# Kernel optimization log

Hardware: AMD Instinct MI355X
Metric: run time of the kernel (lower is better)

The kernel has to match this reference:

```python
import jax, jax.numpy as jnp
import numpy as np

B, N, K, D, H = 32, 4096, 8, 256, 512
ITERS = 3
LN_EPS = 1e-5  # torch LayerNorm default; self.eps is unused in forward


def _ln(x, g, b):
    m = jnp.mean(x, axis=-1, keepdims=True)
    v = jnp.mean(jnp.square(x - m), axis=-1, keepdims=True)
    return (x - m) * jax.lax.rsqrt(v + LN_EPS) * g + b


def setup_inputs() -> dict:
    key = jax.random.key(0)
    ks = jax.random.split(key, 16)
    s = 0.02
    return {
        "inputs": jax.random.normal(ks[0], (B, N, D), jnp.float32),
        "slots_init": jax.random.normal(ks[1], (B, K, D), jnp.float32),
        "ln_in_g": jnp.ones((D,), jnp.float32), "ln_in_b": jnp.zeros((D,), jnp.float32),
        "ln_s_g": jnp.ones((D,), jnp.float32), "ln_s_b": jnp.zeros((D,), jnp.float32),
        "ln_ff_g": jnp.ones((D,), jnp.float32), "ln_ff_b": jnp.zeros((D,), jnp.float32),
        "Wk": s * jax.random.normal(ks[2], (D, D), jnp.float32), "bk": jnp.zeros((D,), jnp.float32),
        "Wq": s * jax.random.normal(ks[3], (D, D), jnp.float32), "bq": jnp.zeros((D,), jnp.float32),
        "Wv": s * jax.random.normal(ks[4], (D, D), jnp.float32), "bv": jnp.zeros((D,), jnp.float32),
        "W_ih": s * jax.random.normal(ks[5], (3 * D, D), jnp.float32),
        "b_ih": jnp.zeros((3 * D,), jnp.float32),
        "W_hh": s * jax.random.normal(ks[6], (3 * D, D), jnp.float32),
        "b_hh": jnp.zeros((3 * D,), jnp.float32),
        "W1": s * jax.random.normal(ks[7], (H, D), jnp.float32), "b1": jnp.zeros((H,), jnp.float32),
        "W2": s * jax.random.normal(ks[8], (D, H), jnp.float32), "b2": jnp.zeros((D,), jnp.float32),
    }


def _gru_cell(x, h, W_ih, b_ih, W_hh, b_hh):
    # PyTorch GRUCell: gates in order r, z, n
    gi = x @ W_ih.T + b_ih  # [*, 3D]
    gh = h @ W_hh.T + b_hh
    ir, iz, inn = jnp.split(gi, 3, axis=-1)
    hr, hz, hn = jnp.split(gh, 3, axis=-1)
    r = jax.nn.sigmoid(ir + hr)
    z = jax.nn.sigmoid(iz + hz)
    n = jnp.tanh(inn + r * hn)
    return (1.0 - z) * n + z * h


def reference(inputs, slots_init, ln_in_g, ln_in_b, ln_s_g, ln_s_b, ln_ff_g, ln_ff_b,
              Wk, bk, Wq, bq, Wv, bv, W_ih, b_ih, W_hh, b_hh, W1, b1, W2, b2):
    d = inputs.shape[-1]
    x = _ln(inputs, ln_in_g, ln_in_b)  # [B,N,D]
    # k, v depend only on x; hoisted out of the loop (same math as source)
    k = x @ Wk.T + bk                  # project_inputs
    v = x @ Wv.T + bv                  # project_v
    scale = 1.0 / jnp.sqrt(jnp.asarray(d, inputs.dtype))
    slots = slots_init
    for _ in range(ITERS):
        slots_prev = slots
        q = _ln(slots, ln_s_g, ln_s_b) @ Wq.T + bq          # [B,K,D]
        attn_logits = jnp.einsum('bkd,bnd->bkn', q, k) * scale
        # competitive softmax over the SLOT axis (dim=1), not keys
        attn = jax.nn.softmax(attn_logits, axis=1)          # [B,K,N]
        updates = jnp.einsum('bkn,bnd->bkd', attn, v)
        slots = _gru_cell(updates, slots_prev, W_ih, b_ih, W_hh, b_hh)
        hdd = jax.nn.relu(_ln(slots, ln_ff_g, ln_ff_b) @ W1.T + b1)
        slots = slots + hdd @ W2.T + b2
    return slots
```

## Files before the change

### kernel.cpp

```cpp
#include <hip/hip_runtime.h>
#include <hip/hip_bf16.h>
#include <cstddef>
#include <cstdint>

#define BB 32
#define NN 4096
#define KK 8
#define DD 256
#define HH 512
#define LN_EPS 1e-5f
#define SCALE 0.0625f
#define NCHUNK 32

__device__ __forceinline__ float wave_sum(float v) {
#pragma unroll
  for (int off = 32; off >= 1; off >>= 1) v += __shfl_xor(v, off);
  return v;
}

__device__ __forceinline__ float sigmoidf_(float x) { return 1.0f / (1.0f + __expf(-x)); }

#define OFF_G   0
#define OFF_W1  393216
#define OFF_W2  524288
#define OFF_WV  655360
#define OFF_WQ  720896
#define OFF_WK  786432
#define WB_ELEMS 851968

#define G_PRE (BB * KK)
#define G_W2B (512 * 11)
#define G_SETUP (G_PRE + G_W2B + 1)

__device__ __forceinline__ float dotp4(uint2 w, float4 s) {
  return __uint_as_float(w.x << 16) * s.x + __uint_as_float(w.x & 0xffff0000u) * s.y +
         __uint_as_float(w.y << 16) * s.z + __uint_as_float(w.y & 0xffff0000u) * s.w;
}

template <int OUT, int KL>
__device__ __forceinline__ float gemv_p(const ushort* __restrict__ wt, int j, int kb,
                                        const float* __restrict__ src) {
  const uint2* p = (const uint2*)(wt + ((size_t)(kb >> 2) * OUT + j) * 4);
  float a = 0.0f;
#pragma unroll 16
  for (int e = 0; e < KL / 4; ++e) {
    uint2 w = p[(size_t)e * OUT];
    float4 s = *(const float4*)(src + kb + e * 4);
    a += dotp4(w, s);
  }
  return a;
}

__global__ __launch_bounds__(256) void k_setup(
    const float* __restrict__ Wih, const float* __restrict__ Whh,
    const float* __restrict__ W1, const float* __restrict__ W2,
    const float* __restrict__ Wv, const float* __restrict__ Wq,
    const float* __restrict__ Wk, ushort* __restrict__ wb,
    const float* __restrict__ slots, const float* __restrict__ gs, const float* __restrict__ bs,
    const float* __restrict__ bq, const float* __restrict__ bk,
    const float* __restrict__ gi, const float* __restrict__ bi,
    const float* __restrict__ bv, float* __restrict__ bvw,
    float* __restrict__ qk, float* __restrict__ qb) {
  int blk = blockIdx.x;
  if (blk < G_PRE) {
    int row = blk;
    int t = threadIdx.x;
    int wid = t >> 6, lane = t & 63;
    __shared__ float lns[DD];
    __shared__ float qs[DD];
    __shared__ float rb[8];
    float sv = slots[(size_t)row * DD + t];
    float s = wave_sum(sv);
    float s2 = wave_sum(sv * sv);
    if (lane == 0) { rb[wid] = s; rb[4 + wid] = s2; }
    __syncthreads();
    float tot = rb[0] + rb[1] + rb[2] + rb[3];
    float tot2 = rb[4] + rb[5] + rb[6] + rb[7];
    float m = tot * (1.0f / DD);
    float var = tot2 * (1.0f / DD) - m * m;
    float rs = rsqrtf(var + LN_EPS);
    lns[t] = (sv - m) * rs * gs[t] + bs[t];
    __syncthreads();
    float acc = 0.0f;
    const float4* wr = (const float4*)(Wq + (size_t)t * DD);
#pragma unroll 4
    for (int e4 = 0; e4 < DD / 4; ++e4) {
      float4 w = wr[e4];
      float4 l = ((const float4*)lns)[e4];
      acc += w.x * l.x + w.y * l.y + w.z * l.z + w.w * l.w;
    }
    qs[t] = acc + bq[t];
    __syncthreads();
    float a2 = 0.0f;
    for (int d = 0; d < DD; ++d) a2 = fmaf(qs[d], Wk[(size_t)d * DD + t], a2);
    float a2S = SCALE * a2;
    qk[(size_t)row * DD + t] = a2S * gi[t];
    float pb = wave_sum(qs[t] * bk[t]);
    float pb2 = wave_sum(a2S * bi[t]);
    __syncthreads();
    if (lane == 0) { rb[wid] = pb; rb[4 + wid] = pb2; }
    __syncthreads();
    if (t == 0) qb[row] = SCALE * (rb[0] + rb[1] + rb[2] + rb[3]) + rb[4] + rb[5] + rb[6] + rb[7];
  } else if (blk < G_PRE + G_W2B) {
    int q2 = blk - G_PRE;
    int m = q2 >> 9;
    int idx = (q2 & 511) * 256 + threadIdx.x;
    const int sizes[11] = {65536, 65536, 65536, 65536, 65536, 65536, 131072, 131072, 65536, 65536, 65536};
    const int offs[11] = {OFF_G, OFF_G + 65536, OFF_G + 131072, OFF_G + 196608, OFF_G + 262144,
                          OFF_G + 327680, OFF_W1, OFF_W2, OFF_WV, OFF_WQ, OFF_WK};
    if (idx >= sizes[m]) return;
    int K = (m == 7) ? 512 : 256;
    int OUT = (m == 6) ? 512 : 256;
    int k = idx % K, j = idx / K;
    float v;
    switch (m) {
      case 0: case 1: case 2: v = Wih[((size_t)(m * 256 + j)) * 256 + k]; break;
      case 3: case 4: case 5: v = Whh[((size_t)((m - 3) * 256 + j)) * 256 + k]; break;
      case 6: v = W1[(size_t)j * 256 + k]; break;
      case 7: v = W2[(size_t)j * 512 + k]; break;
      case 8: v = Wv[(size_t)j * 256 + k] * gi[k]; break;
      case 9: v = Wq[(size_t)j * 256 + k]; break;
      default: v = Wk[(size_t)k * 256 + j]; break;
    }
    __hip_bfloat16 h = __float2bfloat16(v);
    wb[(size_t)offs[m] + (size_t)(k >> 2) * OUT * 4 + j * 4 + (k & 3)] = *(ushort*)&h;
  } else {
    int t = threadIdx.x;
    float a = bv[t];
    const float4* wr = (const float4*)(Wv + (size_t)t * DD);
    const float4* bb = (const float4*)bi;
#pragma unroll 4
    for (int e4 = 0; e4 < DD / 4; ++e4) {
      float4 w = wr[e4];
      float4 x = bb[e4];
      a += w.x * x.x + w.y * x.y + w.z * x.z + w.w * x.w;
    }
    bvw[t] = a;
  }
}

template <int DO_LN>
__global__ __launch_bounds__(256, 2) void k_attn_t(const ushort* __restrict__ xb_in,
                                                   ushort* __restrict__ xb_out,
                                                   const float* __restrict__ inp,
                                                   const float* __restrict__ qk,
                                                   const float* __restrict__ qb,
                                                   float* __restrict__ uxp,
                                                   float* __restrict__ sap) {
  typedef __attribute__((ext_vector_type(8))) short short8;
  typedef __attribute__((ext_vector_type(4))) float f32x4;

  __shared__ __align__(16) ushort q_l[16 * 256];
  __shared__ __align__(16) ushort xt[4][32 * 256];

  int t = threadIdx.x, wid = t >> 6, lane = t & 63;
  int bI = blockIdx.x >> 5, c = blockIdx.x & 31;
  int lm = lane & 15, g = lane >> 4;
  ushort* xw = xt[wid];

  {
    const float* qkb = qk + (size_t)bI * (KK * DD);
#pragma unroll
    for (int s = 0; s < 16; ++s) {
      float qv = qkb[(s & 7) * 256 + t];
      __hip_bfloat16 hb = __float2bfloat16(qv);
      ushort st = *(ushort*)&hb;
      if (s >= 8) {
        float lo = qv - __bfloat162float(hb);
        __hip_bfloat16 lb2 = __float2bfloat16(lo);
        st = *(ushort*)&lb2;
      }
      int pos = (t >> 3) ^ (s & 7);
      q_l[s * 256 + pos * 8 + (t & 7)] = st;
    }
  }
  float qbv = qb[bI * 8 + (lane & 7)];
  __syncthreads();

  int row0 = c * 128 + wid * 32;

  if (DO_LN) {
    int q8 = lane & 7, lr = lane >> 3;
    const float* rp0 = inp + ((size_t)bI * NN + row0 + lr) * DD + q8 * 4;
    float4 cur[8];
#pragma unroll
    for (int i = 0; i < 8; ++i) cur[i] = *(const float4*)(rp0 + i * 32);
    for (int p = 0; p < 4; ++p) {
      float4 nxt[8];
      if (p < 3) {
#pragma unroll
        for (int i = 0; i < 8; ++i) nxt[i] = *(const float4*)(rp0 + (size_t)(p + 1) * 8 * DD + i * 32);
      }
      float s1 = 0.0f, s2 = 0.0f;
#pragma unroll
      for (int i = 0; i < 8; ++i) {
        s1 += cur[i].x + cur[i].y + cur[i].z + cur[i].w;
        s2 += cur[i].x * cur[i].x + cur[i].y * cur[i].y + cur[i].z * cur[i].z + cur[i].w * cur[i].w;
      }
      s1 += __shfl_xor(s1, 1); s2 += __shfl_xor(s2, 1);
      s1 += __shfl_xor(s1, 2); s2 += __shfl_xor(s2, 2);
      s1 += __shfl_xor(s1, 4); s2 += __shfl_xor(s2, 4);
      float m = s1 * (1.0f / DD);
      float var = s2 * (1.0f / DD) - m * m;
      float rs = rsqrtf(var + LN_EPS);
      int rr = p * 8 + lr;
      int hb2 = (q8 & 1) * 4;
#pragma unroll
      for (int i = 0; i < 8; ++i) {
        float y0 = (cur[i].x - m) * rs, y1 = (cur[i].y - m) * rs;
        float y2 = (cur[i].z - m) * rs, y3 = (cur[i].w - m) * rs;
        __hip_bfloat16 h0 = __float2bfloat16(y0), h1 = __float2bfloat16(y1);
        __hip_bfloat16 h2 = __float2bfloat16(y2), h3 = __float2bfloat16(y3);
        uint2 wv;
        wv.x = (uint)*(ushort*)&h0 | ((uint)*(ushort*)&h1 << 16);
        wv.y = (uint)*(ushort*)&h2 | ((uint)*(ushort*)&h3 << 16);
        int chunk = i * 4 + (q8 >> 1);
        *(uint2*)&xw[rr * DD + ((chunk ^ rr) << 3) + hb2] = wv;
      }
      if (p < 3) {
#pragma unroll
        for (int i = 0; i < 8; ++i) cur[i] = nxt[i];
      }
    }
    ushort* xbt = xb_out + ((size_t)bI * NN + row0) * DD;
#pragma unroll
    for (int i = 0; i < 16; ++i) {
      uint4 v = *(const uint4*)&xw[i * 512 + lane * 8];
      *(uint4*)&xbt[i * 512 + lane * 8] = v;
    }
  } else {
    const ushort* srcb = xb_in + ((size_t)bI * NN + row0) * DD;
#pragma unroll
    for (int i = 0; i < 16; ++i) {
      __builtin_amdgcn_global_load_lds(
          (__attribute__((address_space(1))) void*)(srcb + i * 512 + lane * 8),
          (__attribute__((address_space(3))) void*)&xw[i * 512], 16, 0, 0);
    }
    asm volatile("s_waitcnt vmcnt(0)" ::: "memory");
    __builtin_amdgcn_sched_barrier(0);
  }

  union V16 { uint4 u; short8 s; };
  int rA = lm, rB = lm + 16;
  f32x4 ac0 = {}, ac1 = {};
#pragma unroll
  for (int kk = 0; kk < 8; ++kk) {
    V16 qf, x0, x1;
    int ch = kk * 4 + g;
    qf.u = *(const uint4*)&q_l[lm * 256 + ((ch ^ (lm & 7)) << 3)];
    x0.u = *(const uint4*)&xw[rA * 256 + ((ch ^ rA) << 3)];
    x1.u = *(const uint4*)&xw[rB * 256 + ((ch ^ rB) << 3)];
    ac0 = __builtin_amdgcn_mfma_f32_16x16x32_bf16(x0.s, qf.s, ac0, 0, 0, 0);
    ac1 = __builtin_amdgcn_mfma_f32_16x16x32_bf16(x1.s, qf.s, ac1, 0, 0, 0);
  }

  float a0[4], a1[4];
  {
    float lv0[4], lv1[4], mx0[4], mx1[4], ss0[4], ss1[4];
#pragma unroll
    for (int r = 0; r < 4; ++r) {
      lv0[r] = ac0[r] + __shfl_xor(ac0[r], 8) + qbv;
      lv1[r] = ac1[r] + __shfl_xor(ac1[r], 8) + qbv;
      mx0[r] = lv0[r]; mx1[r] = lv1[r];
    }
#pragma unroll
    for (int off = 1; off <= 4; off <<= 1) {
#pragma unroll
      for (int r = 0; r < 4; ++r) {
        mx0[r] = fmaxf(mx0[r], __shfl_xor(mx0[r], off));
        mx1[r] = fmaxf(mx1[r], __shfl_xor(mx1[r], off));
      }
    }
#pragma unroll
    for (int r = 0; r < 4; ++r) {
      a0[r] = __expf(lv0[r] - mx0[r]);
      a1[r] = __expf(lv1[r] - mx1[r]);
      ss0[r] = a0[r]; ss1[r] = a1[r];
    }
#pragma unroll
    for (int off = 1; off <= 4; off <<= 1) {
#pragma unroll
      for (int r = 0; r < 4; ++r) {
        ss0[r] += __shfl_xor(ss0[r], off);
        ss1[r] += __shfl_xor(ss1[r], off);
      }
    }
#pragma unroll
    for (int r = 0; r < 4; ++r) {
      a0[r] *= __frcp_rn(ss0[r]);
      a1[r] *= __frcp_rn(ss1[r]);
    }
  }
  float sacc = 0.0f;
#pragma unroll
  for (int r = 0; r < 4; ++r) sacc += a0[r] + a1[r];
  sacc += __shfl_xor(sacc, 16);
  sacc += __shfl_xor(sacc, 32);

  union A2u { ushort us[8]; short8 s; } au;
  bool lop = (lane & 8) != 0;
#pragma unroll
  for (int e = 0; e < 8; ++e) {
    float av = (e < 4) ? a0[e] : a1[e - 4];
    __hip_bfloat16 hb = __float2bfloat16(av);
    if (lop) {
      float lo = av - __bfloat162float(hb);
      hb = __float2bfloat16(lo);
    }
    au.us[e] = *(ushort*)&hb;
  }

  f32x4 av4[16];
#pragma unroll
  for (int i = 0; i < 16; ++i) av4[i] = (f32x4){0.0f, 0.0f, 0.0f, 0.0f};
#pragma unroll
  for (int dc = 0; dc < 16; ++dc) {
    int d = dc * 16 + lm, dch = d >> 3, d7 = d & 7;
    union A2u bu;
#pragma unroll
    for (int e = 0; e < 4; ++e) {
      int r1 = 4 * g + e;
      int r2 = 16 + 4 * g + e;
      bu.us[e] = xw[r1 * 256 + ((dch ^ r1) << 3) + d7];
      bu.us[4 + e] = xw[r2 * 256 + ((dch ^ r2) << 3) + d7];
    }
    av4[dc] = __builtin_amdgcn_mfma_f32_16x16x32_bf16(au.s, bu.s, av4[dc], 0, 0, 0);
  }

  float* uxwf = (float*)xw;
#pragma unroll
  for (int dc = 0; dc < 16; ++dc) {
#pragma unroll
    for (int r = 0; r < 4; ++r) {
      float v = av4[dc][r];
      float o = v + __shfl_xor(v, 32);
      if (lane < 32) uxwf[(g * 4 + r) * 256 + dc * 16 + lm] = o;
    }
  }
  __syncthreads();
  float* sredf = (float*)q_l;
  if (lane < 8) sredf[wid * 8 + lane] = sacc;
  __syncthreads();
  {
    const float* x0f = (const float*)xt[0];
    const float* x1f = (const float*)xt[1];
    const float* x2f = (const float*)xt[2];
    const float* x3f = (const float*)xt[3];
    size_t obase = ((size_t)(bI * NCHUNK + c)) * (KK * DD);
#pragma unroll
    for (int u = 0; u < 8; ++u) {
      int idx = u * 256 + t;
      uxp[obase + idx] = x0f[idx] + x1f[idx] + x2f[idx] + x3f[idx];
    }
    if (t < 8)
      sap[((size_t)(bI * NCHUNK + c)) * KK + t] =
          sredf[t] + sredf[8 + t] + sredf[16 + t] + sredf[24 + t];
  }
}

__global__ __launch_bounds__(1024) void k_fused(const float* __restrict__ slots_in,
                                                const float* __restrict__ uxp,
                                                const float* __restrict__ sap,
                                                const ushort* __restrict__ wb,
                                                const float* __restrict__ bv,
                                                const float* __restrict__ bih, const float* __restrict__ bhh,
                                                const float* __restrict__ gff, const float* __restrict__ bff,
                                                const float* __restrict__ b1, const float* __restrict__ b2,
                                                const float* __restrict__ gs, const float* __restrict__ bs,
                                                const float* __restrict__ bq, const float* __restrict__ bk,
                                                const float* __restrict__ gi, const float* __restrict__ bi,
                                                float* __restrict__ dst,
                                                float* __restrict__ qk_out,
                                                float* __restrict__ qb_out,
                                                int last) {
  const ushort* WG = wb + OFF_G;
  const ushort* W1p = wb + OFF_W1;
  const ushort* W2p = wb + OFF_W2;
  const ushort* WVp = wb + OFF_WV;
  const ushort* WQp = wb + OFF_WQ;
  const ushort* WKp = wb + OFF_WK;

  __shared__ float ux_s[DD], h_s[DD], upd_s[DD], hn_s[DD], ln_s[DD];
  __shared__ float g_s[6][DD];
  __shared__ float hdd_s[HH];
  __shared__ float tmp4_s[4][DD];
  __shared__ float red_s[16];
  __shared__ float sA_s;
  float* tmpH = &tmp4_s[0][0];

  int t = threadIdx.x, d = t & 255, qr = t >> 8;
  int wid = t >> 6, lane = t & 63;
  int r = blockIdx.x, b = r >> 3, k = r & 7;

  {
    const float* p = uxp + (((size_t)(b * NCHUNK + qr * 8)) * KK + k) * DD + d;
    float s = 0.0f;
#pragma unroll
    for (int i = 0; i < 8; ++i) s += p[(size_t)i * KK * DD];
    tmp4_s[qr][d] = s;
  }
  if (t < 256) h_s[t] = slots_in[(size_t)r * DD + t];
  if (t >= 960) {
    int c = t - 960;
    float v = (c < NCHUNK) ? sap[((size_t)(b * NCHUNK + c)) * KK + k] : 0.0f;
    v = wave_sum(v);
    if (lane == 0) sA_s = v;
  }
  __syncthreads();
  if (t < 256) ux_s[t] = tmp4_s[0][t] + tmp4_s[1][t] + tmp4_s[2][t] + tmp4_s[3][t];
  __syncthreads();

  tmp4_s[qr][d] = gemv_p<256, 64>(WVp, d, qr * 64, ux_s);
  __syncthreads();
  if (t < 256) upd_s[t] = tmp4_s[0][t] + tmp4_s[1][t] + tmp4_s[2][t] + tmp4_s[3][t] + bv[t] * sA_s;
  __syncthreads();

  {
    int g = qr;
    const float* src = (g < 3) ? upd_s : h_s;
    float a = gemv_p<256, 256>(WG + (size_t)g * 65536, d, 0, src);
    g_s[g][d] = a + ((g < 3) ? bih[g * 256 + d] : bhh[d]);
    if (t < 512) {
      int g2 = 4 + (t >> 8), j2 = t & 255;
      float a2 = gemv_p<256, 256>(WG + (size_t)g2 * 65536, j2, 0, h_s);
      g_s[g2][j2] = a2 + bhh[(g2 - 3) * 256 + j2];
    }
  }
  __syncthreads();
  if (t < 256) {
    float rr = sigmoidf_(g_s[0][t] + g_s[3][t]);
    float zz = sigmoidf_(g_s[1][t] + g_s[4][t]);
    float nn = tanhf(g_s[2][t] + rr * g_s[5][t]);
    hn_s[t] = (1.0f - zz) * nn + zz * h_s[t];
  }
  __syncthreads();

  if (t < 256) {
    float v = hn_s[t];
    float sm = wave_sum(v), sq = wave_sum(v * v);
    if (lane == 0) { red_s[wid] = sm; red_s[8 + wid] = sq; }
  }
  __syncthreads();
  if (t < 256) {
    float v = hn_s[t];
    float tot = red_s[0] + red_s[1] + red_s[2] + red_s[3];
    float tot2 = red_s[8] + red_s[9] + red_s[10] + red_s[11];
    float m = tot * (1.0f / DD);
    float var = tot2 * (1.0f / DD) - m * m;
    float rs = rsqrtf(var + LN_EPS);
    ln_s[t] = (v - m) * rs * gff[t] + bff[t];
  }
  __syncthreads();

  {
    int o = t & 511, kh = t >> 9;
    tmpH[kh * 512 + o] = gemv_p<512, 128>(W1p, o, kh * 128, ln_s);
  }
  __syncthreads();
  if (t < 512) hdd_s[t] = fmaxf(tmpH[t] + tmpH[512 + t] + b1[t], 0.0f);
  __syncthreads();

  tmp4_s[qr][d] = gemv_p<256, 128>(W2p, d, qr * 128, hdd_s);
  __syncthreads();
  if (t < 256) {
    float o = hn_s[t] + tmp4_s[0][t] + tmp4_s[1][t] + tmp4_s[2][t] + tmp4_s[3][t] + b2[t];
    dst[(size_t)r * DD + t] = o;
    ux_s[t] = o;
  }
  __syncthreads();

  if (!last) {
    if (t < 256) {
      float v = ux_s[t];
      float sm = wave_sum(v), sq = wave_sum(v * v);
      if (lane == 0) { red_s[wid] = sm; red_s[8 + wid] = sq; }
    }
    __syncthreads();
    if (t < 256) {
      float v = ux_s[t];
      float tot = red_s[0] + red_s[1] + red_s[2] + red_s[3];
      float tot2 = red_s[8] + red_s[9] + red_s[10] + red_s[11];
      float m = tot * (1.0f / DD);
      float var = tot2 * (1.0f / DD) - m * m;
      float rs = rsqrtf(var + LN_EPS);
      ln_s[t] = (v - m) * rs * gs[t] + bs[t];
    }
    __syncthreads();
    tmp4_s[qr][d] = gemv_p<256, 64>(WQp, d, qr * 64, ln_s);
    __syncthreads();
    if (t < 256) {
      float qv = tmp4_s[0][t] + tmp4_s[1][t] + tmp4_s[2][t] + tmp4_s[3][t] + bq[t];
      upd_s[t] = qv;
      float sb = wave_sum(qv * bk[t]);
      if (lane == 0) red_s[wid] = sb;
    }
    __syncthreads();
    {
      float a = gemv_p<256, 64>(WKp, d, qr * 64, upd_s);
      tmp4_s[qr][d] = a;
    }
    __syncthreads();
    if (t < 256) {
      float qkv = SCALE * (tmp4_s[0][t] + tmp4_s[1][t] + tmp4_s[2][t] + tmp4_s[3][t]);
      qk_out[(size_t)r * DD + t] = qkv * gi[t];
      float pb2 = wave_sum(qkv * bi[t]);
      if (lane == 0) red_s[8 + wid] = pb2;
    }
    __syncthreads();
    if (t == 0) qb_out[r] = SCALE * (red_s[0] + red_s[1] + red_s[2] + red_s[3]) +
                            red_s[8] + red_s[9] + red_s[10] + red_s[11];
  }
}

extern "C" void kernel_launch(void* const* d_in, const int* in_sizes, int n_in,
                              void* d_out, int out_size, void* d_ws, size_t ws_size,
                              hipStream_t stream) {
  const float* inputs = (const float*)d_in[0];
  const float* slots_init = (const float*)d_in[1];
  const float* ln_in_g = (const float*)d_in[2];
  const float* ln_in_b = (const float*)d_in[3];
  const float* ln_s_g = (const float*)d_in[4];
  const float* ln_s_b = (const float*)d_in[5];
  const float* ln_ff_g = (const float*)d_in[6];
  const float* ln_ff_b = (const float*)d_in[7];
  const float* Wk = (const float*)d_in[8];
  const float* bk = (const float*)d_in[9];
  const float* Wq = (const float*)d_in[10];
  const float* bq = (const float*)d_in[11];
  const float* Wv = (const float*)d_in[12];
  const float* bv = (const float*)d_in[13];
  const float* Wih = (const float*)d_in[14];
  const float* bih = (const float*)d_in[15];
  const float* Whh = (const float*)d_in[16];
  const float* bhh = (const float*)d_in[17];
  const float* W1 = (const float*)d_in[18];
  const float* b1 = (const float*)d_in[19];
  const float* W2 = (const float*)d_in[20];
  const float* b2 = (const float*)d_in[21];
  float* outp = (float*)d_out;

  char* w = (char*)d_ws;
  ushort* xb = (ushort*)w;       w += (size_t)BB * NN * DD * 2;
  float* qk = (float*)w;         w += (size_t)BB * KK * DD * 4;
  float* qb = (float*)w;         w += (size_t)BB * KK * 4;
  float* uxp = (float*)w;        w += (size_t)BB * NCHUNK * KK * DD * 4;
  float* sap = (float*)w;        w += (size_t)BB * NCHUNK * KK * 4;
  float* slots_ws = (float*)w;   w += (size_t)BB * KK * DD * 4;
  ushort* wb = (ushort*)w;       w += (size_t)WB_ELEMS * 2;
  float* bvw = (float*)w;        w += (size_t)DD * 4;

  k_setup<<<G_SETUP, 256, 0, stream>>>(Wih, Whh, W1, W2, Wv, Wq, Wk, wb,
                                       slots_init, ln_s_g, ln_s_b, bq, bk,
                                       ln_in_g, ln_in_b, bv, bvw, qk, qb);

  for (int it = 0; it < 3; ++it) {
    if (it == 0)
      k_attn_t<1><<<BB * NCHUNK, 256, 0, stream>>>(nullptr, xb, inputs, qk, qb, uxp, sap);
    else
      k_attn_t<0><<<BB * NCHUNK, 256, 0, stream>>>(xb, nullptr, nullptr, qk, qb, uxp, sap);
    const float* sin = (it == 0) ? slots_init : slots_ws;
    float* dst = (it == 2) ? outp : slots_ws;
    k_fused<<<BB * KK, 1024, 0, stream>>>(sin, uxp, sap, wb,
                                          bvw, bih, bhh, ln_ff_g, ln_ff_b, b1, b2,
                                          ln_s_g, ln_s_b, bq, bk, ln_in_g, ln_in_b,
                                          dst, qk, qb, (it == 2) ? 1 : 0);
  }
}
```

Baseline: 234.3 us.

## Re-layout attention LDS tiles chunk-major and overlap LDS-DMA loads with MFMA

```diff
diff --git a/kernel.cpp b/kernel.cpp
--- a/kernel.cpp
+++ b/kernel.cpp
@@ -19,6 +19,11 @@
 }
 
 __device__ __forceinline__ float sigmoidf_(float x) { return 1.0f / (1.0f + __expf(-x)); }
+
+__device__ __forceinline__ uint pk2bf(float x, float y) {
+  __hip_bfloat16 hx = __float2bfloat16(x), hy = __float2bfloat16(y);
+  return (uint)*(ushort*)&hx | ((uint)*(ushort*)&hy << 16);
+}
 
 #define OFF_G   0
 #define OFF_W1  393216
@@ -149,6 +154,7 @@
                                                    float* __restrict__ sap) {
   typedef __attribute__((ext_vector_type(8))) short short8;
   typedef __attribute__((ext_vector_type(4))) float f32x4;
+  union V16 { uint4 u; short8 s; ushort us[8]; };
 
   __shared__ __align__(16) ushort q_l[16 * 256];
   __shared__ __align__(16) ushort xt[4][32 * 256];
@@ -157,40 +163,36 @@
   int bI = blockIdx.x >> 5, c = blockIdx.x & 31;
   int lm = lane & 15, g = lane >> 4;
   ushort* xw = xt[wid];
+  char* xwB = (char*)xw;
+  char* qB = (char*)q_l;
 
   {
     const float* qkb = qk + (size_t)bI * (KK * DD);
-#pragma unroll
-    for (int s = 0; s < 16; ++s) {
-      float qv = qkb[(s & 7) * 256 + t];
+    int p = t >> 3, e7 = t & 7;
+#pragma unroll 1
+    for (int s = 0; s < 8; ++s) {
+      float qv = qkb[s * 256 + t];
       __hip_bfloat16 hb = __float2bfloat16(qv);
-      ushort st = *(ushort*)&hb;
-      if (s >= 8) {
-        float lo = qv - __bfloat162float(hb);
-        __hip_bfloat16 lb2 = __float2bfloat16(lo);
-        st = *(ushort*)&lb2;
-      }
-      int pos = (t >> 3) ^ (s & 7);
-      q_l[s * 256 + pos * 8 + (t & 7)] = st;
+      float lo = qv - __bfloat162float(hb);
+      __hip_bfloat16 lb = __float2bfloat16(lo);
+      *(ushort*)(qB + s * 512 + (((p + s) & 31) << 4) + e7 * 2) = *(ushort*)&hb;
+      *(ushort*)(qB + (s + 8) * 512 + (((p + s + 8) & 31) << 4) + e7 * 2) = *(ushort*)&lb;
     }
   }
   float qbv = qb[bI * 8 + (lane & 7)];
-  __syncthreads();
 
   int row0 = c * 128 + wid * 32;
 
   if (DO_LN) {
+    __syncthreads();
     int q8 = lane & 7, lr = lane >> 3;
     const float* rp0 = inp + ((size_t)bI * NN + row0 + lr) * DD + q8 * 4;
-    float4 cur[8];
-#pragma unroll
-    for (int i = 0; i < 8; ++i) cur[i] = *(const float4*)(rp0 + i * 32);
+    int pb = q8 >> 1, hb8 = (q8 & 1) * 8;
+#pragma unroll 1
     for (int p = 0; p < 4; ++p) {
-      float4 nxt[8];
-      if (p < 3) {
-#pragma unroll
-        for (int i = 0; i < 8; ++i) nxt[i] = *(const float4*)(rp0 + (size_t)(p + 1) * 8 * DD + i * 32);
-      }
+      float4 cur[8];
+#pragma unroll
+      for (int i = 0; i < 8; ++i) cur[i] = *(const float4*)(rp0 + (size_t)p * 8 * DD + i * 32);
       float s1 = 0.0f, s2 = 0.0f;
 #pragma unroll
       for (int i = 0; i < 8; ++i) {
@@ -204,26 +206,16 @@
       float var = s2 * (1.0f / DD) - m * m;
       float rs = rsqrtf(var + LN_EPS);
       int rr = p * 8 + lr;
-      int hb2 = (q8 & 1) * 4;
 #pragma unroll
       for (int i = 0; i < 8; ++i) {
-        float y0 = (cur[i].x - m) * rs, y1 = (cur[i].y - m) * rs;
-        float y2 = (cur[i].z - m) * rs, y3 = (cur[i].w - m) * rs;
-        __hip_bfloat16 h0 = __float2bfloat16(y0), h1 = __float2bfloat16(y1);
-        __hip_bfloat16 h2 = __float2bfloat16(y2), h3 = __float2bfloat16(y3);
         uint2 wv;
-        wv.x = (uint)*(ushort*)&h0 | ((uint)*(ushort*)&h1 << 16);
-        wv.y = (uint)*(ushort*)&h2 | ((uint)*(ushort*)&h3 << 16);
-        int chunk = i * 4 + (q8 >> 1);
-        *(uint2*)&xw[rr * DD + ((chunk ^ rr) << 3) + hb2] = wv;
+        wv.x = pk2bf((cur[i].x - m) * rs, (cur[i].y - m) * rs);
+        wv.y = pk2bf((cur[i].z - m) * rs, (cur[i].w - m) * rs);
+        *(uint2*)(xwB + ((4 * i + pb) << 9) + (rr << 4) + hb8) = wv;
       }
-      if (p < 3) {
-#pragma unroll
-        for (int i = 0; i < 8; ++i) cur[i] = nxt[i];
-      }
     }
     ushort* xbt = xb_out + ((size_t)bI * NN + row0) * DD;
-#pragma unroll
+#pragma unroll 1
     for (int i = 0; i < 16; ++i) {
       uint4 v = *(const uint4*)&xw[i * 512 + lane * 8];
       *(uint4*)&xbt[i * 512 + lane * 8] = v;
@@ -236,20 +228,23 @@
           (__attribute__((address_space(1))) void*)(srcb + i * 512 + lane * 8),
           (__attribute__((address_space(3))) void*)&xw[i * 512], 16, 0, 0);
     }
-    asm volatile("s_waitcnt vmcnt(0)" ::: "memory");
     __builtin_amdgcn_sched_barrier(0);
-  }
-
-  union V16 { uint4 u; short8 s; };
+    asm volatile("s_waitcnt lgkmcnt(0)\n\ts_barrier" ::: "memory");
+    __builtin_amdgcn_sched_barrier(0);
+  }
+
   int rA = lm, rB = lm + 16;
   f32x4 ac0 = {}, ac1 = {};
 #pragma unroll
   for (int kk = 0; kk < 8; ++kk) {
+    if (!DO_LN) {
+      asm volatile("s_waitcnt vmcnt(%0)" ::"i"(14 - 2 * kk) : "memory");
+    }
     V16 qf, x0, x1;
     int ch = kk * 4 + g;
-    qf.u = *(const uint4*)&q_l[lm * 256 + ((ch ^ (lm & 7)) << 3)];
-    x0.u = *(const uint4*)&xw[rA * 256 + ((ch ^ rA) << 3)];
-    x1.u = *(const uint4*)&xw[rB * 256 + ((ch ^ rB) << 3)];
+    qf.u = *(const uint4*)(qB + (lm << 9) + (((ch + lm) & 31) << 4));
+    x0.u = *(const uint4*)(xwB + (ch << 9) + (rA << 4));
+    x1.u = *(const uint4*)(xwB + (ch << 9) + (rB << 4));
     ac0 = __builtin_amdgcn_mfma_f32_16x16x32_bf16(x0.s, qf.s, ac0, 0, 0, 0);
     ac1 = __builtin_amdgcn_mfma_f32_16x16x32_bf16(x1.s, qf.s, ac1, 0, 0, 0);
   }
@@ -297,17 +292,21 @@
   sacc += __shfl_xor(sacc, 16);
   sacc += __shfl_xor(sacc, 32);
 
-  union A2u { ushort us[8]; short8 s; } au;
   bool lop = (lane & 8) != 0;
-#pragma unroll
-  for (int e = 0; e < 8; ++e) {
-    float av = (e < 4) ? a0[e] : a1[e - 4];
-    __hip_bfloat16 hb = __float2bfloat16(av);
-    if (lop) {
-      float lo = av - __bfloat162float(hb);
-      hb = __float2bfloat16(lo);
-    }
-    au.us[e] = *(ushort*)&hb;
+  V16 au;
+  {
+    float t8[8];
+#pragma unroll
+    for (int e = 0; e < 8; ++e) {
+      float av = (e < 4) ? a0[e] : a1[e - 4];
+      if (lop) {
+        __hip_bfloat16 hb = __float2bfloat16(av);
+        av = av - __bfloat162float(hb);
+      }
+      t8[e] = av;
+    }
+    au.u = make_uint4(pk2bf(t8[0], t8[1]), pk2bf(t8[2], t8[3]),
+                      pk2bf(t8[4], t8[5]), pk2bf(t8[6], t8[7]));
   }
 
   f32x4 av4[16];
@@ -315,15 +314,18 @@
   for (int i = 0; i < 16; ++i) av4[i] = (f32x4){0.0f, 0.0f, 0.0f, 0.0f};
 #pragma unroll
   for (int dc = 0; dc < 16; ++dc) {
-    int d = dc * 16 + lm, dch = d >> 3, d7 = d & 7;
-    union A2u bu;
-#pragma unroll
-    for (int e = 0; e < 4; ++e) {
-      int r1 = 4 * g + e;
-      int r2 = 16 + 4 * g + e;
-      bu.us[e] = xw[r1 * 256 + ((dch ^ r1) << 3) + d7];
-      bu.us[4 + e] = xw[r2 * 256 + ((dch ^ r2) << 3) + d7];
-    }
+    int d = dc * 16 + lm, dch = d >> 3, d7b = (d & 7) * 2;
+    int r0 = 4 * g, r2 = 16 + 4 * g;
+    const char* pl = xwB + (dch << 9) + d7b;
+    V16 bu;
+    bu.u.x = (uint)*(const ushort*)(pl + ((r0 + 0) << 4)) |
+             ((uint)*(const ushort*)(pl + ((r0 + 1) << 4)) << 16);
+    bu.u.y = (uint)*(const ushort*)(pl + ((r0 + 2) << 4)) |
+             ((uint)*(const ushort*)(pl + ((r0 + 3) << 4)) << 16);
+    bu.u.z = (uint)*(const ushort*)(pl + ((r2 + 0) << 4)) |
+             ((uint)*(const ushort*)(pl + ((r2 + 1) << 4)) << 16);
+    bu.u.w = (uint)*(const ushort*)(pl + ((r2 + 2) << 4)) |
+             ((uint)*(const ushort*)(pl + ((r2 + 3) << 4)) << 16);
     av4[dc] = __builtin_amdgcn_mfma_f32_16x16x32_bf16(au.s, bu.s, av4[dc], 0, 0, 0);
   }
 
@@ -347,7 +349,7 @@
     const float* x2f = (const float*)xt[2];
     const float* x3f = (const float*)xt[3];
     size_t obase = ((size_t)(bI * NCHUNK + c)) * (KK * DD);
-#pragma unroll
+#pragma unroll 1
     for (int u = 0; u < 8; ++u) {
       int idx = u * 256 + t;
       uxp[obase + idx] = x0f[idx] + x1f[idx] + x2f[idx] + x3f[idx];
```

Measured after the change: 240.0 us. +2.4%, slower.
